# Kernel tuning notes

Hardware: AMD Instinct MI355X
Metric: run time of the kernel (lower is better)

## Reference

```python
import jax, jax.numpy as jnp
from jax import lax
import numpy as np

PS = 3      # patch_size
PROP = 3    # propagate_size
DN = ('NCHW', 'OIHW', 'NCHW')


def _conv1x1(x, W, b):
    # x: [b, c, h, w]; W: [o, c]; 1x1 conv == channel matmul
    return jnp.einsum('oc,bchw->bohw', W, x) + b[None, :, None, None]


def _mpga(q_in, k_in, mask, Wq, bq, Wk, bk, Wv, bv):
    # q_in/k_in: [b, c, w, h], mask: [b, 1, w, h] (already at feature resolution)
    b, c, w, h = q_in.shape
    kp = _conv1x1(k_in, Wk, bk).reshape(b, c, w * h)          # [b, c, wh]
    qp = _conv1x1(q_in, Wq, bq).reshape(b, c, w * h)          # [b, c, wh]
    scores = jnp.einsum('bci,bcj->bij', qp, kp)               # [b, wh_q, wh_k]
    mrow = mask.reshape(b, w * h)[:, :, None]                 # mask over query rows
    A = jax.nn.softmax(scores * mrow, axis=-1)                # softmax over keys
    vp = _conv1x1(k_in, Wv, bv).reshape(b, c, w * h)
    out = jnp.einsum('bcj,bij->bci', vp, A).reshape(b, c, w, h)
    return q_in * mask + (1.0 - mask) * out


def _gap(x, m, Wq, bq, Wk, bk, Wv, bv, gamma):
    # GlobalAttentionPatch on patch stacks: x, m: [N, c, ps, ps]
    N, c, ph, pw = x.shape
    q = jnp.einsum('oc,ncij->noij', Wq, x) + bq[None, :, None, None]
    k = jnp.einsum('oc,ncij->noij', Wk, x) + bk[None, :, None, None]
    v = jnp.einsum('oc,ncij->noij', Wv, x) + bv[None, :, None, None]
    qf, kf, vf, mf = (t.reshape(N, c, ph * pw) for t in (q, k, v, m))
    cc = jnp.einsum('ncp,ndp->ncd', qf, kf)                   # [N, c, c]
    cc = jnp.einsum('ncd,ndp->ncp', cc, mf)                   # [N, c, ps*ps]
    energy = jax.nn.softmax(cc, axis=-1)
    att = (energy * vf).reshape(N, c, ph, pw)
    return x * m + gamma * (1.0 - m) * att


def _patches(x, ps):
    # torch: pad(ps//2) -> unfold(2, ps, 1).unfold(3, ps, 1) -> [b, N=w*h, c, ps, ps]
    b, c, w, h = x.shape
    p = ps // 2
    xp = jnp.pad(x, ((0, 0), (0, 0), (p, p), (p, p)))
    sl = [xp[:, :, di:di + w, dj:dj + h] for di in range(ps) for dj in range(ps)]
    pat = jnp.stack(sl, axis=-1).reshape(b, c, w, h, ps, ps)
    return pat.reshape(b, c, w * h, ps, ps).transpose(0, 2, 1, 3, 4)


def _gla_forward(foreground, mask, pf, pp, gamma):
    background = foreground * (1.0 - mask)
    fg = _mpga(foreground, background, mask, *pf)
    ck_all = _patches(background, PS)                          # [b, N, c, 3, 3]
    mk_all = _patches(jnp.broadcast_to(mask, foreground.shape), PS)
    pad = [(PS // 2, PS // 2)] * 2

    def per_sample(fm, ck, mk):
        # fm: [c, w, h]; ck, mk: [N, c, 3, 3]
        ck = ck + 1e-7
        ck = _gap(ck, mk, *pp, gamma)
        ck = ck / jnp.sqrt(jnp.sum(ck ** 2, axis=(1, 2, 3), keepdims=True))
        cr = lax.conv_general_dilated(fm[None], ck, (1, 1), pad,
                                      dimension_numbers=DN)    # [1, N, w, h]
        N = ck.shape[0]
        prop_k = jnp.ones((N, 1, PROP, PROP), fm.dtype)        # depthwise ones
        cr = lax.conv_general_dilated(cr, prop_k, (1, 1), [(1, 1), (1, 1)],
                                      dimension_numbers=DN, feature_group_count=N)
        mm = (jnp.mean(mk, axis=(1, 2, 3)) == 0.0).astype(fm.dtype)[None, :, None, None]
        att = jax.nn.softmax(cr * mm, axis=1) * mm             # softmax over N patches
        # conv_transpose2d(att, ck, stride=1, padding=1) == conv with flipped, swapped kernel
        Wt = jnp.flip(ck, (2, 3)).transpose(1, 0, 2, 3)        # [c, N, 3, 3]
        rec = lax.conv_general_dilated(att, Wt, (1, 1), pad, dimension_numbers=DN)
        return rec[0]

    return jax.vmap(per_sample)(fg, ck_all, mk_all)


def setup_inputs() -> dict:
    key = jax.random.key(0)
    ks = jax.random.split(key, 8)
    bz, nc, w, h = 2, 64, 64, 64
    s = 0.02
    foreground = jax.random.normal(ks[0], (bz, nc, w, h), jnp.float32)
    mask = jnp.zeros((bz, 1, w, h), jnp.float32).at[:, :, 16:48, 16:48].set(1.0)

    def lin(k):
        kw, kb = jax.random.split(k)
        return (jax.random.normal(kw, (nc, nc), jnp.float32) * s,
                jax.random.normal(kb, (nc,), jnp.float32) * s)

    Wq_f, bq_f = lin(ks[1]); Wk_f, bk_f = lin(ks[2]); Wv_f, bv_f = lin(ks[3])
    Wq_p, bq_p = lin(ks[4]); Wk_p, bk_p = lin(ks[5]); Wv_p, bv_p = lin(ks[6])
    return dict(foreground=foreground, mask=mask, same_number_of_args=0,
                Wq_f=Wq_f, bq_f=bq_f, Wk_f=Wk_f, bk_f=bk_f, Wv_f=Wv_f, bv_f=bv_f,
                Wq_p=Wq_p, bq_p=bq_p, Wk_p=Wk_p, bk_p=bk_p, Wv_p=Wv_p, bv_p=bv_p,
                gamma=jnp.ones((1,), jnp.float32))


def reference(foreground, mask, same_number_of_args,
              Wq_f, bq_f, Wk_f, bk_f, Wv_f, bv_f,
              Wq_p, bq_p, Wk_p, bk_p, Wv_p, bv_p, gamma):
    del same_number_of_args  # unused by the torch module as well
    pf = (Wq_f, bq_f, Wk_f, bk_f, Wv_f, bv_f)
    pp = (Wq_p, bq_p, Wk_p, bk_p, Wv_p, bv_p)
    return _gla_forward(foreground, mask, pf, pp, gamma)
```

## Files before the change

kernel.cpp:

```cpp
#include <hip/hip_runtime.h>


#define BSZ 2
#define C 64
#define WD 64
#define WH 4096
#define PW 66
#define PP 4356
#define KC 576
#define NP 4096

typedef unsigned short u16;
typedef unsigned int u32;
typedef short bf16x8 __attribute__((ext_vector_type(8)));
typedef float f32x4 __attribute__((ext_vector_type(4)));

__device__ inline u16 bf16_rne(float x) {
  unsigned u = __float_as_uint(x);
  return (u16)((u + 0x7FFFu + ((u >> 16) & 1u)) >> 16);
}
__device__ inline float bf16_tof(u16 h) { return __uint_as_float(((unsigned)h) << 16); }
__device__ inline void split2(float x, u16& h, u16& l) {
  h = bf16_rne(x);
  l = bf16_rne(x - bf16_tof(h));
}
__device__ inline u32 pack2(float x) {
  u16 h, l;
  split2(x, h, l);
  return ((u32)h << 16) | (u32)l;
}


__global__ void k_mu(const float* __restrict__ fg, const float* __restrict__ mask,
                     float* __restrict__ mu) {
  int bc = blockIdx.x;
  int b = bc >> 6;
  const float* f = fg + (size_t)bc * WH;
  const float* mk = mask + (size_t)b * WH;
  float sum = 0.f;
  for (int i = threadIdx.x; i < WH; i += 256) sum += f[i] * (1.f - mk[i]);
  __shared__ float red[256];
  red[threadIdx.x] = sum;
  __syncthreads();
  for (int s = 128; s > 0; s >>= 1) {
    if (threadIdx.x < s) red[threadIdx.x] += red[threadIdx.x + s];
    __syncthreads();
  }
  if (threadIdx.x == 0) mu[bc] = red[0] / (float)WH;
}

__global__ void k_vmean(const float* __restrict__ Wv_f, const float* __restrict__ bv_f,
                        const float* __restrict__ mu, float* __restrict__ vmean) {
  int t = threadIdx.x;
  int b = t >> 6, c = t & 63;
  float acc = bv_f[c];
  for (int cc = 0; cc < C; ++cc) acc += Wv_f[c * C + cc] * mu[b * C + cc];
  vmean[t] = acc;
}

__global__ void k_fm(const float* __restrict__ fg, const float* __restrict__ mask,
                     const float* __restrict__ vmean, float* __restrict__ fm) {
  int idx = blockIdx.x * 256 + threadIdx.x;
  if (idx >= BSZ * C * WH) return;
  int b = idx >> 18;
  int c = (idx >> 12) & 63;
  int pos = idx & (WH - 1);
  float m = mask[b * WH + pos];
  fm[idx] = fg[idx] * m + (1.f - m) * vmean[b * C + c];
}

__global__ void k_bgpT(const float* __restrict__ fg, const float* __restrict__ mask,
                       float* __restrict__ bgp) {
  int b = blockIdx.y, xp = blockIdx.x;
  float* out = bgp + ((size_t)b * PP + (size_t)xp * PW) * C;
  int t = threadIdx.x;
  __shared__ float tile[64][65];
  int xi = xp - 1;
  if (xi >= 0 && xi < WD) {
    const float* fgb = fg + (size_t)b * C * WH + (size_t)xi * WD;
    const float* mkb = mask + (size_t)b * WH + (size_t)xi * WD;
    for (int i = t; i < 64 * 64; i += 256) {
      int c = i >> 6, y = i & 63;
      tile[c][y] = fgb[(size_t)c * WH + y] * (1.f - mkb[y]);
    }
  }
  __syncthreads();
  for (int i = t; i < PW * C; i += 256) {
    int yp = i >> 6, c = i & 63;
    float v = 1e-7f;
    int yj = yp - 1;
    if (xi >= 0 && xi < WD && yj >= 0 && yj < WD) v += tile[c][yj];
    out[(size_t)yp * C + c] = v;
  }
}

__global__ void k_vgT(const float* __restrict__ bgp, const float* __restrict__ Wv_p,
                      const float* __restrict__ bv_p, float* __restrict__ Vg) {
  __shared__ float Wt[64][65];
  __shared__ float bgl[4][64];
  int t = threadIdx.x;
  for (int i = t; i < 4096; i += 256) Wt[i & 63][i >> 6] = Wv_p[i];
  int pos0 = blockIdx.x * 4;
  {
    int p2 = t >> 6, c = t & 63;
    int gp = pos0 + p2;
    bgl[p2][c] = (gp < BSZ * PP) ? bgp[(size_t)gp * C + c] : 0.f;
  }
  __syncthreads();
  int pi = t >> 6, o = t & 63;
  int gpos = pos0 + pi;
  if (gpos < BSZ * PP) {
    float acc = bv_p[o];
    for (int c = 0; c < 64; ++c) acc += Wt[c][o] * bgl[pi][c];
    Vg[(size_t)gpos * C + o] = acc;
  }
}

__global__ void k_mmf(const float* __restrict__ mask, float* __restrict__ mmf) {
  int idx = blockIdx.x * 256 + threadIdx.x;
  if (idx >= BSZ * NP) return;
  int b = idx >> 12, n = idx & 4095;
  int x = n >> 6, y = n & 63;
  float z = 0.f;
  for (int di = -1; di <= 1; ++di)
    for (int dj = -1; dj <= 1; ++dj) {
      int xi = x + di, yj = y + dj;
      if (xi >= 0 && xi < WD && yj >= 0 && yj < WD) z += mask[b * WH + xi * WD + yj];
    }
  mmf[idx] = (z == 0.f) ? 1.f : 0.f;
}

__global__ void k_scan(const float* __restrict__ mmf, int* __restrict__ lividx,
                       int* __restrict__ nliv) {
  int b = blockIdx.x, t = threadIdx.x;
  const float* mm = mmf + (size_t)b * NP;
  int* li = lividx + (size_t)b * NP;
  __shared__ int cnt[256];
  int loc[16];
  int c = 0;
#pragma unroll
  for (int i = 0; i < 16; ++i) {
    int lv = (mm[t * 16 + i] != 0.f) ? 1 : 0;
    loc[i] = lv;
    c += lv;
  }
  cnt[t] = c;
  __syncthreads();
  for (int s = 1; s < 256; s <<= 1) {
    int v = (t >= s) ? cnt[t - s] : 0;
    __syncthreads();
    cnt[t] += v;
    __syncthreads();
  }
  int base = cnt[t] - c;
#pragma unroll
  for (int i = 0; i < 16; ++i)
    if (loc[i]) li[base++] = t * 16 + i;
  int nl = cnt[255];
  if (t == 0) nliv[b] = nl;
  for (int i = nl + t; i < NP; i += 256) li[i] = 0;
}

__global__ void k_ck(const float* __restrict__ Vg, const int* __restrict__ lividx,
                     const int* __restrict__ nliv, const float* __restrict__ gamma,
                     u16* __restrict__ AkcH, u16* __restrict__ AkcL) {
  int b = blockIdx.y, nc = blockIdx.x;
  if (nc >= nliv[b]) return;
  int n = lividx[(size_t)b * NP + nc];
  int x = n >> 6, y = n & 63;
  int c = threadIdx.x;
  const float* vg = Vg + (size_t)b * PP * C;
  float g9 = gamma[0] * (1.f / 9.f);
  float o[9];
  float ss = 0.f;
#pragma unroll
  for (int p = 0; p < 9; ++p) {
    int di = p / 3, dj = p % 3;
    float v = g9 * vg[(size_t)((x + di) * PW + (y + dj)) * C + c];
    o[p] = v;
    ss += v * v;
  }
#pragma unroll
  for (int off = 32; off > 0; off >>= 1) ss += __shfl_down(ss, off, 64);
  ss = __shfl(ss, 0, 64);
  float rn = 1.f / sqrtf(ss);
  u16* ph = AkcH + ((size_t)b * NP + nc) * KC + c * 9;
  u16* pl = AkcL + ((size_t)b * NP + nc) * KC + c * 9;
#pragma unroll
  for (int p = 0; p < 9; ++p) {
    u16 h, l;
    split2(o[p] * rn, h, l);
    ph[p] = h;
    pl[p] = l;
  }
}

__global__ void k_trA(const u16* __restrict__ Sh, const u16* __restrict__ Sl,
                      u16* __restrict__ Dh, u16* __restrict__ Dl) {
  __shared__ __align__(16) u16 tile[64][72];
  int x0 = blockIdx.x * 64, k0 = blockIdx.y * 64;
  int t = threadIdx.x;
  for (int pass = 0; pass < 2; ++pass) {
    const u16* S = pass ? Sl : Sh;
    u16* D = pass ? Dl : Dh;
    for (int ch = t; ch < 512; ch += 256) {
      int r = ch >> 3, c0 = (ch & 7) * 8;
      *reinterpret_cast<uint4*>(&tile[r][c0]) =
          *reinterpret_cast<const uint4*>(S + (size_t)(x0 + r) * KC + k0 + c0);
    }
    __syncthreads();
    for (int ch = t; ch < 512; ch += 256) {
      int kr = ch >> 3, c0 = (ch & 7) * 8;
      union { u16 u[8]; uint4 v; } pk;
#pragma unroll
      for (int j = 0; j < 8; ++j) pk.u[j] = tile[c0 + j][kr];
      *reinterpret_cast<uint4*>(D + (size_t)(k0 + kr) * NP + x0 + c0) = pk.v;
    }
    __syncthreads();
  }
}

__global__ void k_im2colT(const float* __restrict__ fm, u16* __restrict__ base) {
  int ch = blockIdx.x * 256 + threadIdx.x;
  if (ch >= BSZ * WH * 72) return;
  int b = ch / (WH * 72);
  int rem = ch - b * WH * 72;
  int xy = rem / 72, kp = rem - xy * 72;
  int x = xy >> 6, y = xy & 63;
  union { u16 u[8]; uint4 v; } H, L;
#pragma unroll
  for (int j = 0; j < 8; ++j) {
    int k = kp * 8 + j;
    int c = k / 9, p = k - c * 9;
    int xi = x + p / 3 - 1, yj = y + p % 3 - 1;
    float v = 0.f;
    if (xi >= 0 && xi < WD && yj >= 0 && yj < WD)
      v = fm[((size_t)(b * C + c)) * WH + (xi << 6) + yj];
    split2(v, H.u[j], L.u[j]);
  }
  u16* bh = base + (size_t)b * 2 * WH * KC;
  u16* bl = bh + (size_t)WH * KC;
  *reinterpret_cast<uint4*>(bh + (size_t)xy * KC + kp * 8) = H.v;
  *reinterpret_cast<uint4*>(bl + (size_t)xy * KC + kp * 8) = L.v;
}


__global__ __launch_bounds__(256, 4) void k_gemmA(
    const u16* __restrict__ Ah, const u16* __restrict__ Al,
    const u16* __restrict__ Bh, const u16* __restrict__ Bl,
    const int* __restrict__ nliv, float* __restrict__ Cp) {
  int nl = *nliv;
  int m0 = blockIdx.y * 128;
  if (m0 >= nl) return;
  int n0 = blockIdx.x * 64;
  __shared__ __align__(16) u16 As[2][128][40];
  __shared__ __align__(16) u16 Bs[2][64][40];
  int t = threadIdx.x;
  f32x4 zero = {0.f, 0.f, 0.f, 0.f};
  f32x4 acc[2][4];
#pragma unroll
  for (int r = 0; r < 2; ++r)
#pragma unroll
    for (int c = 0; c < 4; ++c) acc[r][c] = zero;
  int l = t & 63, w = t >> 6;
  int lr = l & 15, lk = (l >> 4) * 8;
  for (int k0 = 0; k0 < KC; k0 += 32) {
    __syncthreads();
    for (int ch = t; ch < 1536; ch += 256) {
      const u16* src;
      u16* dst;
      if (ch < 1024) {
        int hl = ch >> 9, r = (ch >> 2) & 127, p = ch & 3;
        src = (hl ? Al : Ah) + (size_t)(m0 + r) * KC + k0 + p * 8;
        dst = &As[hl][r][p * 8];
      } else {
        int c2 = ch - 1024;
        int hl = c2 >> 8, r = (c2 >> 2) & 63, p = c2 & 3;
        src = (hl ? Bl : Bh) + (size_t)(n0 + r) * KC + k0 + p * 8;
        dst = &Bs[hl][r][p * 8];
      }
      *reinterpret_cast<uint4*>(dst) = *reinterpret_cast<const uint4*>(src);
    }
    __syncthreads();
    bf16x8 ah[2], al2[2], bh[4], bl2[4];
#pragma unroll
    for (int r = 0; r < 2; ++r) {
      ah[r] = *reinterpret_cast<const bf16x8*>(&As[0][32 * w + 16 * r + lr][lk]);
      al2[r] = *reinterpret_cast<const bf16x8*>(&As[1][32 * w + 16 * r + lr][lk]);
    }
#pragma unroll
    for (int c = 0; c < 4; ++c) {
      bh[c] = *reinterpret_cast<const bf16x8*>(&Bs[0][16 * c + lr][lk]);
      bl2[c] = *reinterpret_cast<const bf16x8*>(&Bs[1][16 * c + lr][lk]);
    }
#pragma unroll
    for (int r = 0; r < 2; ++r)
#pragma unroll
      for (int c = 0; c < 4; ++c) {
        acc[r][c] = __builtin_amdgcn_mfma_f32_16x16x32_bf16(ah[r], bh[c], acc[r][c], 0, 0, 0);
        acc[r][c] = __builtin_amdgcn_mfma_f32_16x16x32_bf16(ah[r], bl2[c], acc[r][c], 0, 0, 0);
        acc[r][c] = __builtin_amdgcn_mfma_f32_16x16x32_bf16(al2[r], bh[c], acc[r][c], 0, 0, 0);
      }
  }
#pragma unroll
  for (int r = 0; r < 2; ++r)
#pragma unroll
    for (int c = 0; c < 4; ++c)
#pragma unroll
      for (int q = 0; q < 4; ++q) {
        int row = m0 + 32 * w + 16 * r + ((l >> 4) << 2) + q;
        Cp[(size_t)row * WH + n0 + 16 * c + lr] = acc[r][c][q];
      }
}

__global__ __launch_bounds__(256, 4) void k_gemmB2(
    const u16* __restrict__ Ah, const u16* __restrict__ Al,
    const u16* __restrict__ Bh, const u16* __restrict__ Bl,
    const int* __restrict__ nliv, float* __restrict__ Cp) {
  int nl = *nliv;
  int Kend = (nl + 31) & ~31;
  int m0 = blockIdx.y * 64;
  int n0 = blockIdx.x * 64;
  __shared__ __align__(16) u16 As[2][64][40];
  __shared__ __align__(16) u16 Bs[2][64][40];
  int t = threadIdx.x;
  f32x4 zero = {0.f, 0.f, 0.f, 0.f};
  f32x4 acc[4];
#pragma unroll
  for (int c = 0; c < 4; ++c) acc[c] = zero;
  int l = t & 63, w = t >> 6;
  int lr = l & 15, lk = (l >> 4) * 8;
  for (int k0 = 0; k0 < Kend; k0 += 32) {
    __syncthreads();
    for (int ch = t; ch < 1024; ch += 256) {
      int sel = ch >> 9;
      int c2 = ch & 511;
      int hl = c2 >> 8, r = (c2 >> 2) & 63, p = c2 & 3;
      const u16* src = sel ? ((hl ? Bl : Bh) + (size_t)(n0 + r) * NP + k0 + p * 8)
                           : ((hl ? Al : Ah) + (size_t)(m0 + r) * NP + k0 + p * 8);
      u16* dst = sel ? &Bs[hl][r][p * 8] : &As[hl][r][p * 8];
      *reinterpret_cast<uint4*>(dst) = *reinterpret_cast<const uint4*>(src);
    }
    __syncthreads();
    bf16x8 ah, al2, bh[4], bl2[4];
    ah = *reinterpret_cast<const bf16x8*>(&As[0][16 * w + lr][lk]);
    al2 = *reinterpret_cast<const bf16x8*>(&As[1][16 * w + lr][lk]);
#pragma unroll
    for (int c = 0; c < 4; ++c) {
      bh[c] = *reinterpret_cast<const bf16x8*>(&Bs[0][16 * c + lr][lk]);
      bl2[c] = *reinterpret_cast<const bf16x8*>(&Bs[1][16 * c + lr][lk]);
    }
#pragma unroll
    for (int c = 0; c < 4; ++c) {
      acc[c] = __builtin_amdgcn_mfma_f32_16x16x32_bf16(ah, bh[c], acc[c], 0, 0, 0);
      acc[c] = __builtin_amdgcn_mfma_f32_16x16x32_bf16(ah, bl2[c], acc[c], 0, 0, 0);
      acc[c] = __builtin_amdgcn_mfma_f32_16x16x32_bf16(al2, bh[c], acc[c], 0, 0, 0);
    }
  }
#pragma unroll
  for (int c = 0; c < 4; ++c)
#pragma unroll
    for (int q = 0; q < 4; ++q) {
      int row = m0 + 16 * w + ((l >> 4) << 2) + q;
      Cp[(size_t)row * WH + n0 + 16 * c + lr] = acc[c][q];
    }
}

__global__ __launch_bounds__(256, 4) void k_gemmB(
    const u16* __restrict__ Ah, const u16* __restrict__ Al,
    const u32* __restrict__ att32, const int* __restrict__ nliv,
    float* __restrict__ Cp) {
  int nl = *nliv;
  int Kend = (nl + 31) & ~31;
  int m0 = blockIdx.y * 64;
  int n0 = blockIdx.x * 64;
  __shared__ __align__(16) u16 As[2][64][40];
  __shared__ __align__(16) u16 Bs[2][64][40];
  __shared__ __align__(16) u32 Bfu[32][70];
  int t = threadIdx.x;
  f32x4 zero = {0.f, 0.f, 0.f, 0.f};
  f32x4 acc[4];
#pragma unroll
  for (int c = 0; c < 4; ++c) acc[c] = zero;
  int l = t & 63, w = t >> 6;
  int lr = l & 15, lk = (l >> 4) * 8;
  for (int k0 = 0; k0 < Kend; k0 += 32) {
    __syncthreads();
    for (int ch = t; ch < 512; ch += 256) {
      int hl = ch >> 8, r = (ch >> 2) & 63, p = ch & 3;
      const u16* src = (hl ? Al : Ah) + (size_t)(m0 + r) * NP + k0 + p * 8;
      *reinterpret_cast<uint4*>(&As[hl][r][p * 8]) = *reinterpret_cast<const uint4*>(src);
    }
    {
      int r = t >> 3, c0 = (t & 7) * 8;
      int krow = k0 + r;
      uint4 w0 = {0u, 0u, 0u, 0u}, w1 = {0u, 0u, 0u, 0u};
      if (krow < nl) {
        const u32* bp = att32 + (size_t)krow * WH + n0 + c0;
        w0 = *reinterpret_cast<const uint4*>(bp);
        w1 = *reinterpret_cast<const uint4*>(bp + 4);
      }
      Bfu[r][c0 + 0] = w0.x; Bfu[r][c0 + 1] = w0.y;
      Bfu[r][c0 + 2] = w0.z; Bfu[r][c0 + 3] = w0.w;
      Bfu[r][c0 + 4] = w1.x; Bfu[r][c0 + 5] = w1.y;
      Bfu[r][c0 + 6] = w1.z; Bfu[r][c0 + 7] = w1.w;
    }
    __syncthreads();
    {
      int n = t >> 2, kq = (t & 3) * 8;
      union { u16 u[8]; uint4 v; } H, L;
#pragma unroll
      for (int j = 0; j < 8; ++j) {
        u32 v = Bfu[kq + j][n];
        H.u[j] = (u16)(v >> 16);
        L.u[j] = (u16)(v & 0xFFFFu);
      }
      *reinterpret_cast<uint4*>(&Bs[0][n][kq]) = H.v;
      *reinterpret_cast<uint4*>(&Bs[1][n][kq]) = L.v;
    }
    __syncthreads();
    bf16x8 ah, al2, bh[4], bl2[4];
    ah = *reinterpret_cast<const bf16x8*>(&As[0][16 * w + lr][lk]);
    al2 = *reinterpret_cast<const bf16x8*>(&As[1][16 * w + lr][lk]);
#pragma unroll
    for (int c = 0; c < 4; ++c) {
      bh[c] = *reinterpret_cast<const bf16x8*>(&Bs[0][16 * c + lr][lk]);
      bl2[c] = *reinterpret_cast<const bf16x8*>(&Bs[1][16 * c + lr][lk]);
    }
#pragma unroll
    for (int c = 0; c < 4; ++c) {
      acc[c] = __builtin_amdgcn_mfma_f32_16x16x32_bf16(ah, bh[c], acc[c], 0, 0, 0);
      acc[c] = __builtin_amdgcn_mfma_f32_16x16x32_bf16(ah, bl2[c], acc[c], 0, 0, 0);
      acc[c] = __builtin_amdgcn_mfma_f32_16x16x32_bf16(al2, bh[c], acc[c], 0, 0, 0);
    }
  }
#pragma unroll
  for (int c = 0; c < 4; ++c)
#pragma unroll
    for (int q = 0; q < 4; ++q) {
      int row = m0 + 16 * w + ((l >> 4) << 2) + q;
      Cp[(size_t)row * WH + n0 + 16 * c + lr] = acc[c][q];
    }
}


__global__ __launch_bounds__(256) void k_box(const int* __restrict__ nliv,
                                             float* __restrict__ cr) {
  if ((int)blockIdx.x >= *nliv) return;
  __shared__ __align__(16) float sIn[WH];
  __shared__ __align__(16) float sT[WH];
  float* row = cr + (size_t)blockIdx.x * WH;
  const float4* r4 = reinterpret_cast<const float4*>(row);
  float4* s4 = reinterpret_cast<float4*>(sIn);
  for (int i = threadIdx.x; i < WH / 4; i += 256) s4[i] = r4[i];
  __syncthreads();
  for (int i = threadIdx.x; i < WH; i += 256) {
    int y = i & 63;
    float v = sIn[i];
    if (y > 0) v += sIn[i - 1];
    if (y < 63) v += sIn[i + 1];
    sT[i] = v;
  }
  __syncthreads();
  for (int i = threadIdx.x; i < WH; i += 256) {
    int x = i >> 6;
    float v = sT[i];
    if (x > 0) v += sT[i - 64];
    if (x < 63) v += sT[i + 64];
    row[i] = v;
  }
}

__global__ __launch_bounds__(256) void k_colstat(const float* __restrict__ cr,
                                                 const int* __restrict__ nliv,
                                                 float* __restrict__ pmax,
                                                 float* __restrict__ psum) {
  int xy = blockIdx.x * 256 + threadIdx.x;
  int nl = *nliv;
  int ns = (nl + 15) >> 4;
  int r0 = blockIdx.y * ns;
  int r1 = min(r0 + ns, nl);
  float mx = -3.4e38f, s = 0.f;
  for (int r = r0; r < r1; ++r) {
    float v = cr[(size_t)r * WH + xy];
    if (v <= mx) {
      s += __expf(v - mx);
    } else {
      s = s * __expf(mx - v) + 1.f;
      mx = v;
    }
  }
  pmax[blockIdx.y * WH + xy] = mx;
  psum[blockIdx.y * WH + xy] = s;
}

__global__ __launch_bounds__(256) void k_colmerge(const int* __restrict__ nliv,
                                                  const float* __restrict__ pmax,
                                                  const float* __restrict__ psum,
                                                  float* __restrict__ m2g,
                                                  float* __restrict__ invg) {
  int xy = blockIdx.x * 256 + threadIdx.x;
  int nl = *nliv;
  float M = -3.4e38f;
  for (int k = 0; k < 16; ++k) M = fmaxf(M, pmax[k * WH + xy]);
  float S = 0.f;
  if (M > -3.0e38f)
    for (int k = 0; k < 16; ++k) S += psum[k * WH + xy] * __expf(pmax[k * WH + xy] - M);
  int nm = NP - nl;
  float m2 = (nm > 0) ? fmaxf(M, 0.f) : M;
  float denom = (M > -3.0e38f ? S * __expf(M - m2) : 0.f) + (float)nm * __expf(-m2);
  m2g[xy] = m2;
  invg[xy] = 1.f / denom;
}

__global__ __launch_bounds__(256) void k_applyT(const int* __restrict__ nliv,
                                                const float* __restrict__ m2g,
                                                const float* __restrict__ invg,
                                                const float* __restrict__ cr,
                                                u16* __restrict__ attT) {
  int nl = *nliv;
  int Kend = (nl + 31) & ~31;
  int n0 = blockIdx.y * 64;
  if (n0 >= Kend) return;
  int x0 = blockIdx.x * 64;
  __shared__ u16 Lh[64][65], Ll[64][65];
  __shared__ float sm2[64], sinv[64];
  int t = threadIdx.x;
  if (t < 64) {
    sm2[t] = m2g[x0 + t];
    sinv[t] = invg[x0 + t];
  }
  __syncthreads();
  for (int e = t; e < 4096; e += 256) {
    int i = e >> 6, j = e & 63;
    float v = 0.f;
    if (n0 + i < nl)
      v = __expf(cr[(size_t)(n0 + i) * WH + x0 + j] - sm2[j]) * sinv[j];
    u16 h, l;
    split2(v, h, l);
    Lh[i][j] = h;
    Ll[i][j] = l;
  }
  __syncthreads();
  u16* p0 = attT;
  u16* p1 = attT + (size_t)WH * NP;
  for (int e = t; e < 4096; e += 256) {
    int a = e >> 6, b2 = e & 63;
    p0[(size_t)(x0 + a) * NP + n0 + b2] = Lh[b2][a];
    p1[(size_t)(x0 + a) * NP + n0 + b2] = Ll[b2][a];
  }
}

__global__ __launch_bounds__(256) void k_apply(const int* __restrict__ nliv,
                                               const float* __restrict__ m2g,
                                               const float* __restrict__ invg,
                                               float* __restrict__ cr) {
  int i = blockIdx.x * 256 + threadIdx.x;
  int row = i >> 10;
  int nl = *nliv;
  int kend = (nl + 31) & ~31;
  if (row >= kend) return;
  float4* p = reinterpret_cast<float4*>(cr) + i;
  uint4* po = reinterpret_cast<uint4*>(cr) + i;
  if (row >= nl) {
    *po = make_uint4(0u, 0u, 0u, 0u);
    return;
  }
  int xy = (i & 1023) << 2;
  float4 v = *p;
  const float4 m2 = *reinterpret_cast<const float4*>(m2g + xy);
  const float4 iv = *reinterpret_cast<const float4*>(invg + xy);
  uint4 o;
  o.x = pack2(__expf(v.x - m2.x) * iv.x);
  o.y = pack2(__expf(v.y - m2.y) * iv.y);
  o.z = pack2(__expf(v.z - m2.z) * iv.z);
  o.w = pack2(__expf(v.w - m2.w) * iv.w);
  *po = o;
}

__global__ void k_rec(const float* __restrict__ P, float* __restrict__ out) {
  int idx = blockIdx.x * 256 + threadIdx.x;
  if (idx >= BSZ * C * WH) return;
  int b = idx >> 18;
  int r = idx & 262143;
  int c = r >> 12;
  int xy = r & 4095;
  int x = xy >> 6, y = xy & 63;
  const float* Pb = P + (size_t)b * KC * WH;
  float acc = 0.f;
#pragma unroll
  for (int i = 0; i < 3; ++i) {
    int xp = x + 1 - i;
    if (xp < 0 || xp >= WD) continue;
#pragma unroll
    for (int j = 0; j < 3; ++j) {
      int yp = y + 1 - j;
      if (yp < 0 || yp >= WD) continue;
      acc += Pb[(size_t)(c * 9 + i * 3 + j) * WH + xp * WD + yp];
    }
  }
  out[idx] = acc;
}


extern "C" void kernel_launch(void* const* d_in, const int* in_sizes, int n_in,
                              void* d_out, int out_size, void* d_ws, size_t ws_size,
                              hipStream_t stream) {
  const float* fg    = (const float*)d_in[0];
  const float* mask  = (const float*)d_in[1];
  const float* Wv_f  = (const float*)d_in[7];
  const float* bv_f  = (const float*)d_in[8];
  const float* Wv_p  = (const float*)d_in[13];
  const float* bv_p  = (const float*)d_in[14];
  const float* gamma = (const float*)d_in[15];

  float* ws = (float*)d_ws;
  size_t off = 0;
  auto alloc = [&](size_t n) { size_t o = off; off += (n + 63) & ~(size_t)63; return o; };
  u16* AkcH = (u16*)(ws + alloc((size_t)BSZ * NP * KC / 2));
  u16* AkcL = (u16*)(ws + alloc((size_t)BSZ * NP * KC / 2));
  u16* AkTH = (u16*)(ws + alloc((size_t)KC * NP / 2));
  u16* AkTL = (u16*)(ws + alloc((size_t)KC * NP / 2));
  float* BimTPb = ws + alloc((size_t)BSZ * KC * WH);
  float* mmf  = ws + alloc((size_t)BSZ * NP);
  int* lividx = (int*)(ws + alloc((size_t)BSZ * NP));
  int* nliv   = (int*)(ws + alloc(64));
  float* mu   = ws + alloc(BSZ * C);
  float* vmn  = ws + alloc(BSZ * C);
  float* pmax = ws + alloc((size_t)16 * WH);
  float* psum = ws + alloc((size_t)16 * WH);
  float* m2g  = ws + alloc(WH);
  float* invg = ws + alloc(WH);
  float* cr   = ws + alloc((size_t)NP * WH);
  size_t attT_off = alloc((size_t)WH * NP);
  float* attT_f = ws + attT_off;
  bool big = (off * sizeof(float)) <= ws_size;
  size_t poff = 0;
  auto palloc = [&](size_t n) { size_t o = poff; poff += (n + 63) & ~(size_t)63; return o; };
  float* bgp = cr + palloc((size_t)BSZ * PP * C);
  float* Vg  = cr + palloc((size_t)BSZ * PP * C);
  float* fmb = cr + palloc((size_t)BSZ * C * WH);
  (void)in_sizes; (void)n_in; (void)out_size;

  k_mu<<<BSZ * C, 256, 0, stream>>>(fg, mask, mu);
  k_vmean<<<1, 128, 0, stream>>>(Wv_f, bv_f, mu, vmn);
  k_fm<<<(BSZ * C * WH + 255) / 256, 256, 0, stream>>>(fg, mask, vmn, fmb);
  k_bgpT<<<dim3(PW, BSZ), 256, 0, stream>>>(fg, mask, bgp);
  k_vgT<<<(BSZ * PP + 3) / 4, 256, 0, stream>>>(bgp, Wv_p, bv_p, Vg);
  k_mmf<<<(BSZ * NP + 255) / 256, 256, 0, stream>>>(mask, mmf);
  k_scan<<<BSZ, 256, 0, stream>>>(mmf, lividx, nliv);
  k_ck<<<dim3(NP, BSZ), 64, 0, stream>>>(Vg, lividx, nliv, gamma, AkcH, AkcL);
  k_im2colT<<<(BSZ * WH * 72 + 255) / 256, 256, 0, stream>>>(fmb, (u16*)BimTPb);

  for (int b = 0; b < BSZ; ++b) {
    const u16* AkcHb = AkcH + (size_t)b * NP * KC;
    const u16* AkcLb = AkcL + (size_t)b * NP * KC;
    const u16* BimTh = (const u16*)BimTPb + (size_t)b * 2 * WH * KC;
    const u16* BimTl = BimTh + (size_t)WH * KC;
    float* Pb = BimTPb + (size_t)b * KC * WH;
    const int* nlb = nliv + b;
    k_trA<<<dim3(NP / 64, KC / 64), 256, 0, stream>>>(AkcHb, AkcLb, AkTH, AkTL);
    k_gemmA<<<dim3(WH / 64, NP / 128), 256, 0, stream>>>(AkcHb, AkcLb, BimTh, BimTl,
                                                         nlb, cr);
    k_box<<<NP, 256, 0, stream>>>(nlb, cr);
    k_colstat<<<dim3(WH / 256, 16), 256, 0, stream>>>(cr, nlb, pmax, psum);
    k_colmerge<<<WH / 256, 256, 0, stream>>>(nlb, pmax, psum, m2g, invg);
    if (big) {
      k_applyT<<<dim3(WH / 64, NP / 64), 256, 0, stream>>>(nlb, m2g, invg, cr,
                                                           (u16*)attT_f);
      k_gemmB2<<<dim3(WH / 64, KC / 64), 256, 0, stream>>>(
          AkTH, AkTL, (u16*)attT_f, (u16*)attT_f + (size_t)WH * NP, nlb, Pb);
    } else {
      k_apply<<<NP * (WH / 4) / 256, 256, 0, stream>>>(nlb, m2g, invg, cr);
      k_gemmB<<<dim3(WH / 64, KC / 64), 256, 0, stream>>>(AkTH, AkTL, (const u32*)cr,
                                                          nlb, Pb);
    }
  }
  k_rec<<<(BSZ * C * WH + 255) / 256, 256, 0, stream>>>(BimTPb, (float*)d_out);
}
```

Baseline: 812.5 us.

## Split-K the second attention GEMM four ways with a separate reduction kernel

The big-path GEMM (attention^T times unfolded keys) is split along K into four z-slices. Each slice writes a partial result into the now-free score buffer, and a new float4 kernel sums the four partials into the output. This exposes four times as many workgroups, which should help a grid of 64x9 tiles that otherwise underfills the GPU on a long K loop. The cost is extra partial-sum writes and reads plus one more launch, and the score buffer must be large enough to hold 4*KC*WH floats.

```diff
diff --git a/kernel.cpp b/kernel.cpp
--- a/kernel.cpp
+++ b/kernel.cpp
@@ -9,6 +9,7 @@
 #define PP 4356
 #define KC 576
 #define NP 4096
+#define SK 4
 
 typedef unsigned short u16;
 typedef unsigned int u32;
@@ -313,12 +314,16 @@
       }
 }
 
-__global__ __launch_bounds__(256, 4) void k_gemmB2(
+__global__ __launch_bounds__(256, 4) void k_gemmB3(
     const u16* __restrict__ Ah, const u16* __restrict__ Al,
     const u16* __restrict__ Bh, const u16* __restrict__ Bl,
-    const int* __restrict__ nliv, float* __restrict__ Cp) {
+    const int* __restrict__ nliv, float* __restrict__ Ppart) {
   int nl = *nliv;
   int Kend = (nl + 31) & ~31;
+  int steps = Kend >> 5;
+  int cs = (steps + SK - 1) / SK;
+  int kbeg = (int)blockIdx.z * cs * 32;
+  int kfin = min(kbeg + cs * 32, Kend);
   int m0 = blockIdx.y * 64;
   int n0 = blockIdx.x * 64;
   __shared__ __align__(16) u16 As[2][64][40];
@@ -330,7 +335,7 @@
   for (int c = 0; c < 4; ++c) acc[c] = zero;
   int l = t & 63, w = t >> 6;
   int lr = l & 15, lk = (l >> 4) * 8;
-  for (int k0 = 0; k0 < Kend; k0 += 32) {
+  for (int k0 = kbeg; k0 < kfin; k0 += 32) {
     __syncthreads();
     for (int ch = t; ch < 1024; ch += 256) {
       int sel = ch >> 9;
@@ -357,6 +362,7 @@
       acc[c] = __builtin_amdgcn_mfma_f32_16x16x32_bf16(al2, bh[c], acc[c], 0, 0, 0);
     }
   }
+  float* Cp = Ppart + (size_t)blockIdx.z * KC * WH;
 #pragma unroll
   for (int c = 0; c < 4; ++c)
 #pragma unroll
@@ -364,6 +370,22 @@
       int row = m0 + 16 * w + ((l >> 4) << 2) + q;
       Cp[(size_t)row * WH + n0 + 16 * c + lr] = acc[c][q];
     }
+}
+
+__global__ __launch_bounds__(256) void k_red4(const float* __restrict__ Pp,
+                                              float* __restrict__ Pb) {
+  int i = blockIdx.x * 256 + threadIdx.x;
+  const float4* p0 = reinterpret_cast<const float4*>(Pp) + i;
+  const float4* p1 = reinterpret_cast<const float4*>(Pp + (size_t)KC * WH) + i;
+  const float4* p2 = reinterpret_cast<const float4*>(Pp + (size_t)2 * KC * WH) + i;
+  const float4* p3 = reinterpret_cast<const float4*>(Pp + (size_t)3 * KC * WH) + i;
+  float4 a = *p0, b = *p1, c = *p2, d = *p3;
+  float4 o;
+  o.x = (a.x + b.x) + (c.x + d.x);
+  o.y = (a.y + b.y) + (c.y + d.y);
+  o.z = (a.z + b.z) + (c.z + d.z);
+  o.w = (a.w + b.w) + (c.w + d.w);
+  *(reinterpret_cast<float4*>(Pb) + i) = o;
 }
 
 __global__ __launch_bounds__(256, 4) void k_gemmB(
@@ -668,8 +690,9 @@
     if (big) {
       k_applyT<<<dim3(WH / 64, NP / 64), 256, 0, stream>>>(nlb, m2g, invg, cr,
                                                            (u16*)attT_f);
-      k_gemmB2<<<dim3(WH / 64, KC / 64), 256, 0, stream>>>(
-          AkTH, AkTL, (u16*)attT_f, (u16*)attT_f + (size_t)WH * NP, nlb, Pb);
+      k_gemmB3<<<dim3(WH / 64, KC / 64, SK), 256, 0, stream>>>(
+          AkTH, AkTL, (u16*)attT_f, (u16*)attT_f + (size_t)WH * NP, nlb, cr);
+      k_red4<<<(KC * WH / 4) / 256, 256, 0, stream>>>(cr, Pb);
     } else {
       k_apply<<<NP * (WH / 4) / 256, 256, 0, stream>>>(nlb, m2g, invg, cr);
       k_gemmB<<<dim3(WH / 64, KC / 64), 256, 0, stream>>>(AkTH, AkTL, (const u32*)cr,
```

Result: faster. 717.6 us (-11.7%).
